# Optimization experiments

Measured on AMD Instinct MI355X. Metric: run time of the kernel, lower is better.

Reference implementation:

```python
import jax, jax.numpy as jnp
import numpy as np

B, R, D, H, C = 256, 100, 6168, 128, 100  # batch, replicas, in_dim, hidden, classes


def setup_inputs() -> dict:
    key = jax.random.key(0)
    k1, k2, k3, k4, k5, k6 = jax.random.split(key, 6)
    # binary input features (texas dataset is binary; original casts to bool)
    x = jax.random.randint(k1, (B, D), 0, 2).astype(jnp.int32)
    # Bernoulli(0.5) flip mask, one per replica per feature
    noise = jax.random.randint(k2, (B, R, D), 0, 2).astype(jnp.int32)
    s1 = 1.0 / np.sqrt(D)
    W1 = jax.random.uniform(k3, (D, H), minval=-s1, maxval=s1, dtype=jnp.float32)
    b1 = jax.random.uniform(k4, (H,), minval=-s1, maxval=s1, dtype=jnp.float32)
    s2 = 1.0 / np.sqrt(H)
    W2 = jax.random.uniform(k5, (H, C), minval=-s2, maxval=s2, dtype=jnp.float32)
    b2 = jax.random.uniform(k6, (C,), minval=-s2, maxval=s2, dtype=jnp.float32)
    return {"x": x, "noise": noise, "W1": W1, "b1": b1, "W2": W2, "b2": b2}


def reference(x, noise, W1, b1, W2, b2):
    # np.invert(x, where=noise) on booleans == flip bit where noise==1
    xb = x[:, None, :]                                   # [B,1,D]
    x_noisy = jnp.where(noise == 1, 1 - xb, xb).astype(W1.dtype)  # [B,R,D]
    h = jnp.tanh(jnp.einsum('brd,dh->brh', x_noisy, W1) + b1)      # [B,R,H]
    logits = jnp.einsum('brh,hc->brc', h, W2) + b2                 # [B,R,C]
    return logits.mean(axis=1)                                     # [B,C]
```

## Files before the change

### kernel.cpp

```cpp
#include <hip/hip_runtime.h>
#include <hip/hip_bf16.h>

#define NB 256
#define NR 100
#define ND 6168
#define DP 6272
#define NH 128
#define NC 100
#define NW 196
#define ROWW 196
#define ROWB 784
#define BITS_B (NR * ROWB)
#define CPR 25
#define TOTAL_CHUNKS (NB * NR * CPR)
#define W1T_BYTES ((size_t)NH * DP * 2)
#define XBITS_BYTES ((size_t)NB * ROWW * 4 + 1024)

#define L_XB 0
#define L_BITS 1024
#define L_TOT (1024 + 77 * 1024)

typedef __attribute__((ext_vector_type(8))) __bf16 bf16x8;
typedef __attribute__((ext_vector_type(4))) float f32x4;
typedef __attribute__((ext_vector_type(4))) int i32x4;
typedef __attribute__((ext_vector_type(4))) unsigned int u32x4;
typedef unsigned int u32;
typedef unsigned long long u64;

typedef const __attribute__((address_space(1))) u32* gas_ptr;
typedef __attribute__((address_space(3))) u32* las_ptr;

__device__ __forceinline__ void gload16(const void* g, void* l) {
  __builtin_amdgcn_global_load_lds((gas_ptr)g, (las_ptr)l, 16, 0, 0);
}

__global__ void prep_w1t(const float* __restrict__ W1, __hip_bfloat16* __restrict__ W1T) {
  __shared__ float tile[32][NH + 1];
  const int d0 = blockIdx.x * 32;
  const int t = threadIdx.x;
#pragma unroll
  for (int p = 0; p < 16; ++p) {
    int idx = p * 256 + t;
    int dd = idx >> 7;
    int h  = idx & 127;
    int d  = d0 + dd;
    tile[dd][h] = (d < ND) ? W1[d * NH + h] : 0.f;
  }
  __syncthreads();
#pragma unroll
  for (int p = 0; p < 16; ++p) {
    int idx = p * 256 + t;
    int h  = idx >> 5;
    int dd = idx & 31;
    int sd = (dd & 7) * 4 + (dd >> 3);
    W1T[h * DP + d0 + dd] = __float2bfloat16(tile[sd][h]);
  }
}

#define PACK_CHUNK(SRCBASE, K0, DSTROW, WJBASE)                                \
  do {                                                                         \
    int kc = ((K0) + 4 <= ND) ? (K0) : (ND - 4);                               \
    i32x4 v = *(const i32x4*)((SRCBASE) + kc);                                 \
    u64 M0 = __ballot((v[0] & 1) != 0);                                        \
    u64 M1 = __ballot((v[1] & 1) != 0);                                        \
    u64 M2 = __ballot((v[2] & 1) != 0);                                        \
    u64 M3 = __ballot((v[3] & 1) != 0);                                        \
    if (lane < 8) {                                                            \
      int wj = (WJBASE) + lane;                                                \
      if (wj < ROWW) {                                                         \
        int sh = 8 * lane;                                                     \
        u32 b0 = (u32)(M0 >> sh) & 0xffu;                                      \
        u32 b1 = (u32)(M1 >> sh) & 0xffu;                                      \
        u32 b2 = (u32)(M2 >> sh) & 0xffu;                                      \
        u32 b3 = (u32)(M3 >> sh) & 0xffu;                                      \
        (DSTROW)[wj] = b0 | (b1 << 8) | (b2 << 16) | (b3 << 24);               \
      }                                                                        \
    }                                                                          \
  } while (0)

__global__ void prep_xbits(const int* __restrict__ x, u32* __restrict__ xbits) {
  const int b    = blockIdx.x;
  const int lane = threadIdx.x & 63;
  const int wv   = threadIdx.x >> 6;
  const int* src = x + (size_t)b * ND;
  u32* dst = xbits + (size_t)b * ROWW;
  for (int c = wv; c < CPR; c += 4)
    PACK_CHUNK(src, c * 256 + lane * 4, dst, c * 8);
}

__global__ void pack_noise(const int* __restrict__ noise, u32* __restrict__ bits) {
  const int lane = threadIdx.x & 63;
  const int wv   = threadIdx.x >> 6;
  for (int cw = blockIdx.x * 4 + wv; cw < TOTAL_CHUNKS; cw += 8192) {
    const int row = cw / CPR;
    const int c   = cw - row * CPR;
    const int* src = noise + (size_t)row * ND;
    u32* dst = bits + (size_t)row * ROWW;
    PACK_CHUNK(src, c * 256 + lane * 4, dst, c * 8);
  }
}

__launch_bounds__(512, 1)
__global__ void gemm(const u32* __restrict__ bits, const __hip_bfloat16* __restrict__ W1T,
                     const float* __restrict__ b1, const u32* __restrict__ xbits,
                     const float* __restrict__ W2, const float* __restrict__ b2,
                     float* __restrict__ out) {
  __shared__ __align__(16) char lds[L_TOT];
  const int tid  = threadIdx.x;
  const int lane = tid & 63;
  const int w    = tid >> 6;
  const int wm   = w >> 2;
  const int wn   = w & 3;
  const int lq   = lane >> 4;
  const int lm   = lane & 15;
  const int b    = blockIdx.x;

  {
    const char* bb = (const char*)bits + (size_t)b * BITS_B;
    for (int c = w; c < 77; c += 8) {
      u32 off = (u32)(c * 1024 + lane * 16);
      if (off > BITS_B - 16) off = BITS_B - 16;
      gload16(bb + off, lds + L_BITS + c * 1024);
    }
    if (w == 0) gload16((const char*)(xbits + (size_t)b * ROWW) + lane * 16, lds + L_XB);
  }
  __syncthreads();

  f32x4 acc[4][2] = {};
  int rcb[4];
#pragma unroll
  for (int mf = 0; mf < 4; ++mf) {
    int row = wm * 64 + mf * 16 + lm;
    rcb[mf] = ((row < NR) ? row : (NR - 1)) * ROWB;
  }
  const __hip_bfloat16* wsrcA = W1T + (size_t)(wn * 32 + lm) * DP + lq * 8;
  const __hip_bfloat16* wsrcB = W1T + (size_t)(wn * 32 + 16 + lm) * DP + lq * 8;
  const int lsh = lq * 8;

  auto BLOAD = [&](int t, bf16x8* Br) {
    Br[0] = *(const bf16x8*)(wsrcA + t * 32);
    Br[1] = *(const bf16x8*)(wsrcB + t * 32);
  };
  auto CONS = [&](int t, const bf16x8* Br) {
    u32 xw = *(const u32*)(lds + L_XB + t * 4);
#pragma unroll
    for (int mf = 0; mf < 4; ++mf) {
      u32 word = (*(const u32*)(lds + L_BITS + rcb[mf] + t * 4)) ^ xw;
      u32 by = (word >> lsh) & 0xffu;
      u32 p0 = ((by & 1u)  ? 0x3F80u : 0u) | ((by & 2u)   ? 0x3F800000u : 0u);
      u32 p1 = ((by & 4u)  ? 0x3F80u : 0u) | ((by & 8u)   ? 0x3F800000u : 0u);
      u32 p2 = ((by & 16u) ? 0x3F80u : 0u) | ((by & 32u)  ? 0x3F800000u : 0u);
      u32 p3 = ((by & 64u) ? 0x3F80u : 0u) | ((by & 128u) ? 0x3F800000u : 0u);
      u32x4 pk = {p0, p1, p2, p3};
      bf16x8 af = *(bf16x8*)&pk;
      acc[mf][0] = __builtin_amdgcn_mfma_f32_16x16x32_bf16(af, Br[0], acc[mf][0], 0, 0, 0);
      acc[mf][1] = __builtin_amdgcn_mfma_f32_16x16x32_bf16(af, Br[1], acc[mf][1], 0, 0, 0);
    }
  };

  bf16x8 Bc[2], Bn[2];
  BLOAD(0, Bc);
#pragma unroll 1
  for (int t = 0; t < NW; t += 2) {
    BLOAD(t + 1, Bn);
    CONS(t, Bc);
    BLOAD((t + 2 < NW) ? (t + 2) : (NW - 1), Bc);
    CONS(t + 1, Bn);
  }

  __syncthreads();
  float* hpart = (float*)lds;
  float* hbar  = (float*)(lds + 1024);
#pragma unroll
  for (int nf = 0; nf < 2; ++nf) {
    int hcol = wn * 32 + nf * 16 + lm;
    float bb = b1[hcol];
    float ssum = 0.f;
#pragma unroll
    for (int mf = 0; mf < 4; ++mf) {
#pragma unroll
      for (int rg = 0; rg < 4; ++rg) {
        int m = wm * 64 + mf * 16 + lq * 4 + rg;
        float tv = tanhf(acc[mf][nf][rg] + bb);
        ssum += (m < NR) ? tv : 0.f;
      }
    }
    ssum += __shfl_xor(ssum, 16, 64);
    ssum += __shfl_xor(ssum, 32, 64);
    if (lq == 0) hpart[wm * 128 + hcol] = ssum;
  }
  __syncthreads();
  if (tid < NH) hbar[tid] = (hpart[tid] + hpart[128 + tid]) * (1.0f / NR);
  __syncthreads();
  if (tid < NC) {
    float sacc = b2[tid];
#pragma unroll 8
    for (int h = 0; h < NH; ++h) sacc += hbar[h] * W2[h * NC + tid];
    out[b * NC + tid] = sacc;
  }
}

extern "C" void kernel_launch(void* const* d_in, const int* in_sizes, int n_in,
                              void* d_out, int out_size, void* d_ws, size_t ws_size,
                              hipStream_t stream) {
  (void)in_sizes; (void)n_in; (void)out_size; (void)ws_size;
  const int* x     = (const int*)d_in[0];
  const int* noise = (const int*)d_in[1];
  const float* W1  = (const float*)d_in[2];
  const float* b1  = (const float*)d_in[3];
  const float* W2  = (const float*)d_in[4];
  const float* b2  = (const float*)d_in[5];
  float* out = (float*)d_out;

  __hip_bfloat16* W1T = (__hip_bfloat16*)d_ws;
  u32* xbits = (u32*)((char*)d_ws + W1T_BYTES);
  u32* bits  = (u32*)((char*)d_ws + W1T_BYTES + XBITS_BYTES);

  prep_w1t<<<DP / 32, 256, 0, stream>>>(W1, W1T);
  prep_xbits<<<NB, 256, 0, stream>>>(x, xbits);
  pack_noise<<<2048, 256, 0, stream>>>(noise, bits);
  gemm<<<NB, 512, 0, stream>>>(bits, W1T, b1, xbits, W2, b2, out);
}
```

Baseline: 249.1 us.

## Fuse input and noise bit-packing into the GEMM kernel

```diff
diff --git a/kernel.cpp b/kernel.cpp
--- a/kernel.cpp
+++ b/kernel.cpp
@@ -10,15 +10,13 @@
 #define NW 196
 #define ROWW 196
 #define ROWB 784
-#define BITS_B (NR * ROWB)
 #define CPR 25
-#define TOTAL_CHUNKS (NB * NR * CPR)
+#define NCHUNK (NR * CPR)
 #define W1T_BYTES ((size_t)NH * DP * 2)
-#define XBITS_BYTES ((size_t)NB * ROWW * 4 + 1024)
 
 #define L_XB 0
 #define L_BITS 1024
-#define L_TOT (1024 + 77 * 1024)
+#define L_TOT (1024 + NR * ROWB)
 
 typedef __attribute__((ext_vector_type(8))) __bf16 bf16x8;
 typedef __attribute__((ext_vector_type(4))) float f32x4;
@@ -27,13 +25,6 @@
 typedef unsigned int u32;
 typedef unsigned long long u64;
 
-typedef const __attribute__((address_space(1))) u32* gas_ptr;
-typedef __attribute__((address_space(3))) u32* las_ptr;
-
-__device__ __forceinline__ void gload16(const void* g, void* l) {
-  __builtin_amdgcn_global_load_lds((gas_ptr)g, (las_ptr)l, 16, 0, 0);
-}
-
 __global__ void prep_w1t(const float* __restrict__ W1, __hip_bfloat16* __restrict__ W1T) {
   __shared__ float tile[32][NH + 1];
   const int d0 = blockIdx.x * 32;
@@ -57,55 +48,15 @@
   }
 }
 
-#define PACK_CHUNK(SRCBASE, K0, DSTROW, WJBASE)                                \
-  do {                                                                         \
-    int kc = ((K0) + 4 <= ND) ? (K0) : (ND - 4);                               \
-    i32x4 v = *(const i32x4*)((SRCBASE) + kc);                                 \
-    u64 M0 = __ballot((v[0] & 1) != 0);                                        \
-    u64 M1 = __ballot((v[1] & 1) != 0);                                        \
-    u64 M2 = __ballot((v[2] & 1) != 0);                                        \
-    u64 M3 = __ballot((v[3] & 1) != 0);                                        \
-    if (lane < 8) {                                                            \
-      int wj = (WJBASE) + lane;                                                \
-      if (wj < ROWW) {                                                         \
-        int sh = 8 * lane;                                                     \
-        u32 b0 = (u32)(M0 >> sh) & 0xffu;                                      \
-        u32 b1 = (u32)(M1 >> sh) & 0xffu;                                      \
-        u32 b2 = (u32)(M2 >> sh) & 0xffu;                                      \
-        u32 b3 = (u32)(M3 >> sh) & 0xffu;                                      \
-        (DSTROW)[wj] = b0 | (b1 << 8) | (b2 << 16) | (b3 << 24);               \
-      }                                                                        \
-    }                                                                          \
-  } while (0)
-
-__global__ void prep_xbits(const int* __restrict__ x, u32* __restrict__ xbits) {
-  const int b    = blockIdx.x;
-  const int lane = threadIdx.x & 63;
-  const int wv   = threadIdx.x >> 6;
-  const int* src = x + (size_t)b * ND;
-  u32* dst = xbits + (size_t)b * ROWW;
-  for (int c = wv; c < CPR; c += 4)
-    PACK_CHUNK(src, c * 256 + lane * 4, dst, c * 8);
-}
-
-__global__ void pack_noise(const int* __restrict__ noise, u32* __restrict__ bits) {
-  const int lane = threadIdx.x & 63;
-  const int wv   = threadIdx.x >> 6;
-  for (int cw = blockIdx.x * 4 + wv; cw < TOTAL_CHUNKS; cw += 8192) {
-    const int row = cw / CPR;
-    const int c   = cw - row * CPR;
-    const int* src = noise + (size_t)row * ND;
-    u32* dst = bits + (size_t)row * ROWW;
-    PACK_CHUNK(src, c * 256 + lane * 4, dst, c * 8);
-  }
-}
-
 __launch_bounds__(512, 1)
-__global__ void gemm(const u32* __restrict__ bits, const __hip_bfloat16* __restrict__ W1T,
-                     const float* __restrict__ b1, const u32* __restrict__ xbits,
-                     const float* __restrict__ W2, const float* __restrict__ b2,
-                     float* __restrict__ out) {
+__global__ void fused(const int* __restrict__ x, const int* __restrict__ noise,
+                      const __hip_bfloat16* __restrict__ W1T,
+                      const float* __restrict__ b1, const float* __restrict__ W2,
+                      const float* __restrict__ b2, float* __restrict__ out) {
   __shared__ __align__(16) char lds[L_TOT];
+  u32* xb_lds   = (u32*)(lds + L_XB);
+  u32* bits_lds = (u32*)(lds + L_BITS);
+
   const int tid  = threadIdx.x;
   const int lane = tid & 63;
   const int w    = tid >> 6;
@@ -116,13 +67,68 @@
   const int b    = blockIdx.x;
 
   {
-    const char* bb = (const char*)bits + (size_t)b * BITS_B;
-    for (int c = w; c < 77; c += 8) {
-      u32 off = (u32)(c * 1024 + lane * 16);
-      if (off > BITS_B - 16) off = BITS_B - 16;
-      gload16(bb + off, lds + L_BITS + c * 1024);
-    }
-    if (w == 0) gload16((const char*)(xbits + (size_t)b * ROWW) + lane * 16, lds + L_XB);
+    const int* xsrc = x + (size_t)b * ND;
+#pragma unroll
+    for (int j = 0; j < 4; ++j) {
+      int c = w * 4 + j;
+      if (c < CPR) {
+        int k0 = c * 256 + lane * 4;
+        int kc = (k0 + 4 <= ND) ? k0 : (ND - 4);
+        i32x4 v = *(const i32x4*)(xsrc + kc);
+        u64 M0 = __ballot((v[0] & 1) != 0);
+        u64 M1 = __ballot((v[1] & 1) != 0);
+        u64 M2 = __ballot((v[2] & 1) != 0);
+        u64 M3 = __ballot((v[3] & 1) != 0);
+        if (lane < 8) {
+          int wj = c * 8 + lane;
+          if (wj < ROWW) {
+            int sh = 8 * lane;
+            u32 c0 = (u32)(M0 >> sh) & 0xffu;
+            u32 c1 = (u32)(M1 >> sh) & 0xffu;
+            u32 c2 = (u32)(M2 >> sh) & 0xffu;
+            u32 c3 = (u32)(M3 >> sh) & 0xffu;
+            xb_lds[wj] = c0 | (c1 << 8) | (c2 << 16) | (c3 << 24);
+          }
+        }
+      }
+    }
+  }
+  {
+    const int* nsrc = noise + (size_t)b * NR * ND;
+#pragma unroll 1
+    for (int i = 0; i < (NCHUNK + 31) / 32; ++i) {
+      i32x4 v[4];
+      int rr[4], cc[4];
+#pragma unroll
+      for (int j = 0; j < 4; ++j) {
+        int q = i * 32 + w * 4 + j;
+        q = (q < NCHUNK) ? q : (NCHUNK - 1);
+        int r = q / CPR;
+        int c = q - r * CPR;
+        rr[j] = r; cc[j] = c;
+        int k0 = c * 256 + lane * 4;
+        int kc = (k0 + 4 <= ND) ? k0 : (ND - 4);
+        v[j] = *(const i32x4*)(nsrc + (size_t)r * ND + kc);
+      }
+#pragma unroll
+      for (int j = 0; j < 4; ++j) {
+        u64 M0 = __ballot((v[j][0] & 1) != 0);
+        u64 M1 = __ballot((v[j][1] & 1) != 0);
+        u64 M2 = __ballot((v[j][2] & 1) != 0);
+        u64 M3 = __ballot((v[j][3] & 1) != 0);
+        if (lane < 8) {
+          int wj = cc[j] * 8 + lane;
+          if (wj < ROWW) {
+            int sh = 8 * lane;
+            u32 c0 = (u32)(M0 >> sh) & 0xffu;
+            u32 c1 = (u32)(M1 >> sh) & 0xffu;
+            u32 c2 = (u32)(M2 >> sh) & 0xffu;
+            u32 c3 = (u32)(M3 >> sh) & 0xffu;
+            bits_lds[rr[j] * ROWW + wj] = c0 | (c1 << 8) | (c2 << 16) | (c3 << 24);
+          }
+        }
+      }
+    }
   }
   __syncthreads();
 
@@ -213,11 +219,7 @@
   float* out = (float*)d_out;
 
   __hip_bfloat16* W1T = (__hip_bfloat16*)d_ws;
-  u32* xbits = (u32*)((char*)d_ws + W1T_BYTES);
-  u32* bits  = (u32*)((char*)d_ws + W1T_BYTES + XBITS_BYTES);
 
   prep_w1t<<<DP / 32, 256, 0, stream>>>(W1, W1T);
-  prep_xbits<<<NB, 256, 0, stream>>>(x, xbits);
-  pack_noise<<<2048, 256, 0, stream>>>(noise, bits);
-  gemm<<<NB, 512, 0, stream>>>(bits, W1T, b1, xbits, W2, b2, out);
+  fused<<<NB, 512, 0, stream>>>(x, noise, W1T, b1, W2, b2, out);
 }
```

Result: faster. 223.1 us (-10.5%).
